# Kernel optimization log

Measured on AMD Instinct MI355X. Metric: run time of the kernel, lower is better.

Reference implementation:

```python
import jax, jax.numpy as jnp
import numpy as np
import math

B, I, O, SEG = 128, 2048, 2048, 10

def setup_inputs() -> dict:
    key = jax.random.key(0)
    k1, k2, k3, k4 = jax.random.split(key, 4)
    scale = 1.0 / math.sqrt(I)
    return {
        "x": jax.random.normal(k1, (B, I), dtype=jnp.float32),
        "context": jax.random.normal(k2, (O,), dtype=jnp.float32),
        "prev_activation": jax.random.normal(k3, (B, O), dtype=jnp.float32),
        "weight": jax.random.normal(k4, (O, I), dtype=jnp.float32) * scale,
        "bias": jnp.zeros((O,), dtype=jnp.float32),
        "astrocyte_activation": jnp.ones((O,), dtype=jnp.float32),
        "dendrite_segments": jax.random.normal(jax.random.fold_in(key, 7), (O, I, SEG), dtype=jnp.float32) * scale,
    }

def reference(x, context, prev_activation, weight, bias, astrocyte_activation, dendrite_segments):
    # Astrocyte gating of the linear weight: sigmoid(astro * context) -> [o]
    astro_mod = jax.nn.sigmoid(astrocyte_activation * context)
    # Dendritic branch: relu(einsum('bi,oij->boj')) summed over segments -> [b, o]
    dendritic_out = jnp.maximum(jnp.einsum('bi,oij->boj', x, dendrite_segments), 0.0).sum(axis=2)
    # Gated linear: F.linear(x, weight * astro_mod[:, None], bias) -> [b, o]
    out = x @ (weight * astro_mod[:, None]).T + bias
    # Note: torch's STDP/Hebbian weight mutations (synaptic_tag, protein_synthesis,
    # homeostatic scaling) occur AFTER 'out' is computed and do not affect the
    # returned tensor; they are pure parameter side effects, so omitted here.
    return out + dendritic_out
```

## Files before the change

### kernel.cpp

```cpp
#include <hip/hip_runtime.h>
#include <hip/hip_bf16.h>

#define B_ 128
#define I_ 2048
#define O_ 2048
#define SEG 10
#define BK 64
#define NST (I_ / BK)
#define XTILE 16384
#define DCH 2560
#define DLS 2816

typedef __attribute__((ext_vector_type(8))) short bf16x8;
typedef __attribute__((ext_vector_type(4))) float f32x4;

static __device__ __forceinline__ unsigned short f2bf(float f) {
    unsigned u = __float_as_uint(f);
    u += 0x7FFFu + ((u >> 16) & 1u);
    return (unsigned short)(u >> 16);
}

#define GLDS16(SRC, DST) \
    __builtin_amdgcn_global_load_lds( \
        (const __attribute__((address_space(1))) unsigned*)(SRC), \
        (__attribute__((address_space(3))) unsigned*)(DST), 16, 0, 0)
#define GLDS4(SRC, DST) \
    __builtin_amdgcn_global_load_lds( \
        (const __attribute__((address_space(1))) unsigned*)(SRC), \
        (__attribute__((address_space(3))) unsigned*)(DST), 4, 0, 0)

__global__ void xconv(const float* __restrict__ x, char* __restrict__ xb) {
    int idx = blockIdx.x * 256 + threadIdx.x;
    int row = idx >> 8;
    int c   = idx & 255;
    int k0  = c * 8;
    int t   = k0 >> 6;
    int kl  = k0 & 63;

    const float* xp = x + (size_t)row * I_ + k0;
    float4 a = *reinterpret_cast<const float4*>(xp);
    float4 b = *reinterpret_cast<const float4*>(xp + 4);

    bf16x8 h;
    h[0] = (short)f2bf(a.x); h[1] = (short)f2bf(a.y);
    h[2] = (short)f2bf(a.z); h[3] = (short)f2bf(a.w);
    h[4] = (short)f2bf(b.x); h[5] = (short)f2bf(b.y);
    h[6] = (short)f2bf(b.z); h[7] = (short)f2bf(b.w);

    size_t off = (size_t)t * XTILE + row * 128 + ((kl * 2) ^ ((row & 7) << 4));
    *reinterpret_cast<bf16x8*>(xb + off) = h;
}

__global__ __launch_bounds__(256, 2) void neuro_fused(
    const char*  __restrict__ xb,
    const float* __restrict__ ctx,
    const float* __restrict__ w,
    const float* __restrict__ bias,
    const float* __restrict__ astro,
    const float* __restrict__ D,
    float* __restrict__ out)
{
    __shared__ __align__(16) char xs[2][XTILE];
    __shared__ __align__(16) char dls[4][2][DLS];

    const int tid  = threadIdx.x;
    const int wave = tid >> 6;
    const int lane = tid & 63;
    const int o    = blockIdx.x * 4 + wave;
    const int col  = lane & 15;
    const int g    = lane >> 4;

    f32x4 acc[8];
#pragma unroll
    for (int m = 0; m < 8; ++m) acc[m] = (f32x4){0.f, 0.f, 0.f, 0.f};

    float am = astro[o] * ctx[o];
    am = 1.0f / (1.0f + __expf(-am));
    const float bo = bias[o];

    const int   fbase = (col < 10) ? col * 4 : DCH;
    const int   fstr  = (col < 10) ? 40 : 4;
    const float dmask = (col <= 10) ? 1.0f : 0.0f;
    const int   sw    = (col & 7) << 4;

    auto stage_x = [&](int t, int buf) {
        const char* src = xb + (size_t)t * XTILE + wave * 4096 + lane * 16;
        char* dst = &xs[buf][wave * 4096];
#pragma unroll
        for (int c = 0; c < 4; ++c)
            GLDS16(src + c * 1024, dst + c * 1024);
    };

    auto stage_d = [&](int t, int buf) {
        const char* srcD = (const char*)D + (size_t)o * (I_ * SEG * 4) + (size_t)t * DCH;
        char* dst = &dls[wave][buf][0];
#pragma unroll
        for (int c = 0; c < 2; ++c)
            GLDS16(srcD + c * 1024 + lane * 16, dst + c * 1024);
#pragma unroll
        for (int c = 0; c < 2; ++c)
            GLDS4(srcD + 2048 + c * 256 + lane * 4, dst + 2048 + c * 256);
        const char* srcW = (const char*)w + (size_t)o * (I_ * 4) + t * (BK * 4);
        GLDS4(srcW + lane * 4, dst + DCH);
    };

    auto compute = [&](int buf) {
        const char* dbase = &dls[wave][buf][0];
        const char* xbase = &xs[buf][0];
#pragma unroll
        for (int kk = 0; kk < 2; ++kk) {
            const char* fp = dbase + fbase + (32 * kk + 8 * g) * fstr;
            bf16x8 bfrag;
#pragma unroll
            for (int e = 0; e < 8; ++e) {
                float v = *reinterpret_cast<const float*>(fp + e * fstr);
                bfrag[e] = (short)f2bf(v * dmask);
            }
            const int kswz = (64 * kk + 16 * g) ^ sw;
#pragma unroll
            for (int m = 0; m < 8; ++m) {
                bf16x8 afrag = *reinterpret_cast<const bf16x8*>(
                    xbase + (m * 16 + col) * 128 + kswz);
                acc[m] = __builtin_amdgcn_mfma_f32_16x16x32_bf16(afrag, bfrag, acc[m], 0, 0, 0);
            }
        }
    };

    stage_x(0, 0);
    stage_d(0, 0);
    __syncthreads();

#pragma unroll 1
    for (int t = 0; t < NST; t += 2) {
        stage_x(t + 1, 1);
        stage_d(t + 1, 1);
        compute(0);
        __syncthreads();

        if (t + 2 < NST) {
            stage_x(t + 2, 0);
            stage_d(t + 2, 0);
        }
        compute(1);
        __syncthreads();
    }

#pragma unroll
    for (int m = 0; m < 8; ++m) {
#pragma unroll
        for (int r = 0; r < 4; ++r) {
            float v = acc[m][r];
            float dend = (col < 10) ? fmaxf(v, 0.0f) : 0.0f;
#pragma unroll
            for (int s = 1; s < 16; s <<= 1)
                dend += __shfl_xor(dend, s, 64);
            float lin = __shfl(v, (lane & 48) | 10, 64);
            if (col == 0) {
                int b = m * 16 + g * 4 + r;
                out[(size_t)b * O_ + o] = dend + am * lin + bo;
            }
        }
    }
}

extern "C" void kernel_launch(void* const* d_in, const int* in_sizes, int n_in,
                              void* d_out, int out_size, void* d_ws, size_t ws_size,
                              hipStream_t stream) {
    const float* x     = (const float*)d_in[0];
    const float* ctx   = (const float*)d_in[1];
    const float* w     = (const float*)d_in[3];
    const float* bias  = (const float*)d_in[4];
    const float* astro = (const float*)d_in[5];
    const float* D     = (const float*)d_in[6];
    float* out = (float*)d_out;
    char* xb = (char*)d_ws;

    xconv<<<dim3(128), dim3(256), 0, stream>>>(x, xb);
    neuro_fused<<<dim3(O_ / 4), dim3(256), 0, stream>>>(xb, ctx, w, bias, astro, D, out);
}
```

Measured before the change: 51.88 us.

## Split K across wave pairs, each wave computing two outputs to reuse x fragments

Each block still covers 4 output neurons, but each wave now handles 2 neurons over half of the K dimension (split-K with 2 slices). A-fragments are loaded once per stage and reused across both neurons, and the two K-halves are combined through LDS at the end. The aim is fewer LDS reads of x per MFMA and a different memory-level parallelism pattern. In exchange the tile is halved to BK=32 with a new swizzle, the accumulator register count doubles, and a cross-wave reduction step is added.

```diff
diff --git a/kernel.cpp b/kernel.cpp
--- a/kernel.cpp
+++ b/kernel.cpp
@@ -5,11 +5,12 @@
 #define I_ 2048
 #define O_ 2048
 #define SEG 10
-#define BK 64
-#define NST (I_ / BK)
-#define XTILE 16384
-#define DCH 2560
-#define DLS 2816
+#define BK 32
+#define KSLICE 1024
+#define NST (KSLICE / BK)
+#define XTILE 8192
+#define DCH 1280
+#define DLS 1408
 
 typedef __attribute__((ext_vector_type(8))) short bf16x8;
 typedef __attribute__((ext_vector_type(4))) float f32x4;
@@ -34,8 +35,8 @@
     int row = idx >> 8;
     int c   = idx & 255;
     int k0  = c * 8;
-    int t   = k0 >> 6;
-    int kl  = k0 & 63;
+    int tt  = k0 >> 5;
+    int kl  = k0 & 31;
 
     const float* xp = x + (size_t)row * I_ + k0;
     float4 a = *reinterpret_cast<const float4*>(xp);
@@ -47,7 +48,8 @@
     h[4] = (short)f2bf(b.x); h[5] = (short)f2bf(b.y);
     h[6] = (short)f2bf(b.z); h[7] = (short)f2bf(b.w);
 
-    size_t off = (size_t)t * XTILE + row * 128 + ((kl * 2) ^ ((row & 7) << 4));
+    int sw = ((row >> 1) & 3) << 4;
+    size_t off = (size_t)tt * XTILE + row * 64 + ((kl * 2) ^ sw);
     *reinterpret_cast<bf16x8*>(xb + off) = h;
 }
 
@@ -60,69 +62,69 @@
     const float* __restrict__ D,
     float* __restrict__ out)
 {
-    __shared__ __align__(16) char xs[2][XTILE];
-    __shared__ __align__(16) char dls[4][2][DLS];
+    __shared__ __align__(16) char xs[2][2][XTILE];
+    __shared__ __align__(16) char dls[4][2][2][DLS];
 
     const int tid  = threadIdx.x;
     const int wave = tid >> 6;
     const int lane = tid & 63;
-    const int o    = blockIdx.x * 4 + wave;
+    const int p    = wave >> 1;
+    const int s    = wave & 1;
+    const int o0   = blockIdx.x * 4 + p * 2;
     const int col  = lane & 15;
     const int g    = lane >> 4;
 
-    f32x4 acc[8];
-#pragma unroll
-    for (int m = 0; m < 8; ++m) acc[m] = (f32x4){0.f, 0.f, 0.f, 0.f};
-
-    float am = astro[o] * ctx[o];
-    am = 1.0f / (1.0f + __expf(-am));
-    const float bo = bias[o];
+    f32x4 acc[2][8];
+#pragma unroll
+    for (int oo = 0; oo < 2; ++oo)
+#pragma unroll
+        for (int m = 0; m < 8; ++m) acc[oo][m] = (f32x4){0.f, 0.f, 0.f, 0.f};
 
     const int   fbase = (col < 10) ? col * 4 : DCH;
     const int   fstr  = (col < 10) ? 40 : 4;
     const float dmask = (col <= 10) ? 1.0f : 0.0f;
-    const int   sw    = (col & 7) << 4;
+    const int   sw    = ((col >> 1) & 3) << 4;
 
     auto stage_x = [&](int t, int buf) {
-        const char* src = xb + (size_t)t * XTILE + wave * 4096 + lane * 16;
-        char* dst = &xs[buf][wave * 4096];
+        const char* src = xb + (size_t)(s * NST + t) * XTILE + p * 4096 + lane * 16;
+        char* dst = &xs[s][buf][p * 4096];
 #pragma unroll
         for (int c = 0; c < 4; ++c)
             GLDS16(src + c * 1024, dst + c * 1024);
     };
 
     auto stage_d = [&](int t, int buf) {
-        const char* srcD = (const char*)D + (size_t)o * (I_ * SEG * 4) + (size_t)t * DCH;
-        char* dst = &dls[wave][buf][0];
-#pragma unroll
-        for (int c = 0; c < 2; ++c)
-            GLDS16(srcD + c * 1024 + lane * 16, dst + c * 1024);
-#pragma unroll
-        for (int c = 0; c < 2; ++c)
-            GLDS4(srcD + 2048 + c * 256 + lane * 4, dst + 2048 + c * 256);
-        const char* srcW = (const char*)w + (size_t)o * (I_ * 4) + t * (BK * 4);
-        GLDS4(srcW + lane * 4, dst + DCH);
+        const size_t krow = (size_t)(s * KSLICE + t * BK);
+#pragma unroll
+        for (int oo = 0; oo < 2; ++oo) {
+            const char* srcD = (const char*)D + ((size_t)(o0 + oo) * (I_ * SEG) + krow * SEG) * 4;
+            char* dst = &dls[wave][buf][oo][0];
+            GLDS16(srcD + lane * 16, dst);
+            GLDS4(srcD + 1024 + lane * 4, dst + 1024);
+            const char* srcW = (const char*)w + ((size_t)(o0 + oo) * I_ + krow) * 4;
+            if (lane < 32) GLDS4(srcW + lane * 4, dst + DCH);
+        }
     };
 
     auto compute = [&](int buf) {
-        const char* dbase = &dls[wave][buf][0];
-        const char* xbase = &xs[buf][0];
-#pragma unroll
-        for (int kk = 0; kk < 2; ++kk) {
-            const char* fp = dbase + fbase + (32 * kk + 8 * g) * fstr;
+        const char* xbase = &xs[s][buf][0];
+        bf16x8 af[8];
+#pragma unroll
+        for (int m = 0; m < 8; ++m)
+            af[m] = *reinterpret_cast<const bf16x8*>(
+                xbase + (m * 16 + col) * 64 + ((16 * g) ^ sw));
+#pragma unroll
+        for (int oo = 0; oo < 2; ++oo) {
+            const char* fp = &dls[wave][buf][oo][0] + fbase + (8 * g) * fstr;
             bf16x8 bfrag;
 #pragma unroll
             for (int e = 0; e < 8; ++e) {
                 float v = *reinterpret_cast<const float*>(fp + e * fstr);
                 bfrag[e] = (short)f2bf(v * dmask);
             }
-            const int kswz = (64 * kk + 16 * g) ^ sw;
-#pragma unroll
-            for (int m = 0; m < 8; ++m) {
-                bf16x8 afrag = *reinterpret_cast<const bf16x8*>(
-                    xbase + (m * 16 + col) * 128 + kswz);
-                acc[m] = __builtin_amdgcn_mfma_f32_16x16x32_bf16(afrag, bfrag, acc[m], 0, 0, 0);
-            }
+#pragma unroll
+            for (int m = 0; m < 8; ++m)
+                acc[oo][m] = __builtin_amdgcn_mfma_f32_16x16x32_bf16(af[m], bfrag, acc[oo][m], 0, 0, 0);
         }
     };
 
@@ -145,19 +147,37 @@
         __syncthreads();
     }
 
-#pragma unroll
-    for (int m = 0; m < 8; ++m) {
-#pragma unroll
-        for (int r = 0; r < 4; ++r) {
-            float v = acc[m][r];
-            float dend = (col < 10) ? fmaxf(v, 0.0f) : 0.0f;
-#pragma unroll
-            for (int s = 1; s < 16; s <<= 1)
-                dend += __shfl_xor(dend, s, 64);
-            float lin = __shfl(v, (lane & 48) | 10, 64);
-            if (col == 0) {
-                int b = m * 16 + g * 4 + r;
-                out[(size_t)b * O_ + o] = dend + am * lin + bo;
+    float* cs = reinterpret_cast<float*>(&xs[0][0][0]);
+    if (s == 1) {
+#pragma unroll
+        for (int oo = 0; oo < 2; ++oo)
+#pragma unroll
+            for (int m = 0; m < 8; ++m)
+                *reinterpret_cast<f32x4*>(cs + p * 4096 + (oo * 8 + m) * 256 + lane * 4) = acc[oo][m];
+    }
+    __syncthreads();
+    if (s == 0) {
+#pragma unroll
+        for (int oo = 0; oo < 2; ++oo) {
+            float am = astro[o0 + oo] * ctx[o0 + oo];
+            am = 1.0f / (1.0f + __expf(-am));
+            const float bo = bias[o0 + oo];
+#pragma unroll
+            for (int m = 0; m < 8; ++m) {
+                f32x4 other = *reinterpret_cast<const f32x4*>(cs + p * 4096 + (oo * 8 + m) * 256 + lane * 4);
+#pragma unroll
+                for (int r = 0; r < 4; ++r) {
+                    float v = acc[oo][m][r] + other[r];
+                    float dend = (col < 10) ? fmaxf(v, 0.0f) : 0.0f;
+#pragma unroll
+                    for (int sh = 1; sh < 16; sh <<= 1)
+                        dend += __shfl_xor(dend, sh, 64);
+                    float lin = __shfl(v, (lane & 48) | 10, 64);
+                    if (col == 0) {
+                        int b = m * 16 + g * 4 + r;
+                        out[(size_t)b * O_ + (o0 + oo)] = dend + am * lin + bo;
+                    }
+                }
             }
         }
     }
@@ -176,5 +196,5 @@
     char* xb = (char*)d_ws;
 
     xconv<<<dim3(128), dim3(256), 0, stream>>>(x, xb);
-    neuro_fused<<<dim3(O_ / 4), dim3(256), 0, stream>>>(xb, ctx, w, bias, astro, D, out);
-}
+    neuro_fused<<<dim3(512), dim3(256), 0, stream>>>(xb, ctx, w, bias, astro, D, out);
+}
```

After: 54.72 us. 1.05x slower.

## Pre-pack weight to bf16 and restructure D/x/w staging into separate pipelines

Applied to the files above, without the earlier changes.

Adds a wpack kernel that converts the linear weight to bf16 and interleaves four output rows per group, so the main kernel loads it with 16-byte async LDS copies instead of 4-byte ones. Dendrite segments are now staged in 5 KB chunks covering two K-steps, using only 16-byte copies, and the weight is staged once every four steps by a single wave. The main loop becomes one step per iteration with separate prefetch cadences for x, D and w. The cost is an extra kernel launch and a weight conversion pass on every call, plus a column-dependent branch when building the B fragment.

```diff
diff --git a/kernel.cpp b/kernel.cpp
--- a/kernel.cpp
+++ b/kernel.cpp
@@ -6,10 +6,10 @@
 #define O_ 2048
 #define SEG 10
 #define BK 64
-#define NST (I_ / BK)
+#define NT (I_ / BK)
+#define NSS (I_ / 128)
 #define XTILE 16384
-#define DCH 2560
-#define DLS 2816
+#define DSS 5120
 
 typedef __attribute__((ext_vector_type(8))) short bf16x8;
 typedef __attribute__((ext_vector_type(4))) float f32x4;
@@ -24,17 +24,13 @@
     __builtin_amdgcn_global_load_lds( \
         (const __attribute__((address_space(1))) unsigned*)(SRC), \
         (__attribute__((address_space(3))) unsigned*)(DST), 16, 0, 0)
-#define GLDS4(SRC, DST) \
-    __builtin_amdgcn_global_load_lds( \
-        (const __attribute__((address_space(1))) unsigned*)(SRC), \
-        (__attribute__((address_space(3))) unsigned*)(DST), 4, 0, 0)
 
 __global__ void xconv(const float* __restrict__ x, char* __restrict__ xb) {
     int idx = blockIdx.x * 256 + threadIdx.x;
     int row = idx >> 8;
     int c   = idx & 255;
     int k0  = c * 8;
-    int t   = k0 >> 6;
+    int tt  = k0 >> 6;
     int kl  = k0 & 63;
 
     const float* xp = x + (size_t)row * I_ + k0;
@@ -47,21 +43,38 @@
     h[4] = (short)f2bf(b.x); h[5] = (short)f2bf(b.y);
     h[6] = (short)f2bf(b.z); h[7] = (short)f2bf(b.w);
 
-    size_t off = (size_t)t * XTILE + row * 128 + ((kl * 2) ^ ((row & 7) << 4));
+    size_t off = (size_t)tt * XTILE + row * 128 + ((kl * 2) ^ ((row & 7) << 4));
     *reinterpret_cast<bf16x8*>(xb + off) = h;
+}
+
+__global__ void wpack(const float* __restrict__ w, char* __restrict__ wp) {
+    int idx = blockIdx.x * 256 + threadIdx.x;
+    int grp = idx >> 10;
+    int kc2 = idx & 1023;
+
+    bf16x8 h;
+#pragma unroll
+    for (int ol = 0; ol < 4; ++ol) {
+        float2 v = *reinterpret_cast<const float2*>(
+            w + ((size_t)(grp * 4 + ol)) * I_ + kc2 * 2);
+        h[ol]     = (short)f2bf(v.x);
+        h[4 + ol] = (short)f2bf(v.y);
+    }
+    *reinterpret_cast<bf16x8*>(wp + (size_t)grp * 16384 + kc2 * 16) = h;
 }
 
 __global__ __launch_bounds__(256, 2) void neuro_fused(
     const char*  __restrict__ xb,
+    const char*  __restrict__ wp,
     const float* __restrict__ ctx,
-    const float* __restrict__ w,
     const float* __restrict__ bias,
     const float* __restrict__ astro,
     const float* __restrict__ D,
     float* __restrict__ out)
 {
     __shared__ __align__(16) char xs[2][XTILE];
-    __shared__ __align__(16) char dls[4][2][DLS];
+    __shared__ __align__(16) char dD[4][2][DSS];
+    __shared__ __align__(16) char wb[2][2048];
 
     const int tid  = threadIdx.x;
     const int wave = tid >> 6;
@@ -78,71 +91,83 @@
     am = 1.0f / (1.0f + __expf(-am));
     const float bo = bias[o];
 
-    const int   fbase = (col < 10) ? col * 4 : DCH;
-    const int   fstr  = (col < 10) ? 40 : 4;
-    const float dmask = (col <= 10) ? 1.0f : 0.0f;
-    const int   sw    = (col & 7) << 4;
-
-    auto stage_x = [&](int t, int buf) {
+    const char* Dbase = (const char*)D + (size_t)o * (I_ * SEG * 4);
+    const int sw = (col & 7) << 4;
+
+    auto stage_x = [&](int t) {
         const char* src = xb + (size_t)t * XTILE + wave * 4096 + lane * 16;
-        char* dst = &xs[buf][wave * 4096];
+        char* dst = &xs[t & 1][wave * 4096];
 #pragma unroll
         for (int c = 0; c < 4; ++c)
             GLDS16(src + c * 1024, dst + c * 1024);
     };
 
-    auto stage_d = [&](int t, int buf) {
-        const char* srcD = (const char*)D + (size_t)o * (I_ * SEG * 4) + (size_t)t * DCH;
-        char* dst = &dls[wave][buf][0];
-#pragma unroll
-        for (int c = 0; c < 2; ++c)
-            GLDS16(srcD + c * 1024 + lane * 16, dst + c * 1024);
-#pragma unroll
-        for (int c = 0; c < 2; ++c)
-            GLDS4(srcD + 2048 + c * 256 + lane * 4, dst + 2048 + c * 256);
-        const char* srcW = (const char*)w + (size_t)o * (I_ * 4) + t * (BK * 4);
-        GLDS4(srcW + lane * 4, dst + DCH);
-    };
-
-    auto compute = [&](int buf) {
-        const char* dbase = &dls[wave][buf][0];
-        const char* xbase = &xs[buf][0];
+    auto stage_D = [&](int S) {
+        const char* src = Dbase + (size_t)S * DSS + lane * 16;
+        char* dst = &dD[wave][S & 1][0];
+#pragma unroll
+        for (int c = 0; c < 5; ++c)
+            GLDS16(src + c * 1024, dst + c * 1024);
+    };
+
+    auto stage_w = [&](int g4) {
+        if (wave == (g4 & 3)) {
+            const char* src = wp + (size_t)blockIdx.x * 16384 + g4 * 2048 + lane * 16;
+            char* dst = &wb[g4 & 1][0];
+            GLDS16(src, dst);
+            GLDS16(src + 1024, dst + 1024);
+        }
+    };
+
+    auto compute = [&](int t) {
+        const char* xbase = &xs[t & 1][0];
+        const char* dbase = &dD[wave][(t >> 1) & 1][(t & 1) * 2560];
+        const char* wbase = &wb[(t >> 2) & 1][0];
 #pragma unroll
         for (int kk = 0; kk < 2; ++kk) {
-            const char* fp = dbase + fbase + (32 * kk + 8 * g) * fstr;
             bf16x8 bfrag;
-#pragma unroll
-            for (int e = 0; e < 8; ++e) {
-                float v = *reinterpret_cast<const float*>(fp + e * fstr);
-                bfrag[e] = (short)f2bf(v * dmask);
+            if (col < 10) {
+                const char* fp = dbase + kk * 1280 + (8 * g) * 40 + col * 4;
+#pragma unroll
+                for (int e = 0; e < 8; ++e)
+                    bfrag[e] = (short)f2bf(*reinterpret_cast<const float*>(fp + e * 40));
+            } else if (col == 10) {
+                const char* fp = wbase + ((t & 3) * 64 + kk * 32 + 8 * g) * 8 + wave * 2;
+#pragma unroll
+                for (int e = 0; e < 8; ++e)
+                    bfrag[e] = *reinterpret_cast<const short*>(fp + e * 8);
+            } else {
+#pragma unroll
+                for (int e = 0; e < 8; ++e) bfrag[e] = 0;
             }
-            const int kswz = (64 * kk + 16 * g) ^ sw;
+            const int kswz = (kk * 64 + 16 * g) ^ sw;
 #pragma unroll
             for (int m = 0; m < 8; ++m) {
-                bf16x8 afrag = *reinterpret_cast<const bf16x8*>(
+                bf16x8 af = *reinterpret_cast<const bf16x8*>(
                     xbase + (m * 16 + col) * 128 + kswz);
-                acc[m] = __builtin_amdgcn_mfma_f32_16x16x32_bf16(afrag, bfrag, acc[m], 0, 0, 0);
+                acc[m] = __builtin_amdgcn_mfma_f32_16x16x32_bf16(af, bfrag, acc[m], 0, 0, 0);
             }
         }
     };
 
-    stage_x(0, 0);
-    stage_d(0, 0);
-    __syncthreads();
+    stage_x(0); stage_x(1);
+    stage_D(0); stage_D(1);
+    stage_w(0); stage_w(1);
 
 #pragma unroll 1
-    for (int t = 0; t < NST; t += 2) {
-        stage_x(t + 1, 1);
-        stage_d(t + 1, 1);
-        compute(0);
+    for (int t = 0; t < NT; ++t) {
         __syncthreads();
-
-        if (t + 2 < NST) {
-            stage_x(t + 2, 0);
-            stage_d(t + 2, 0);
-        }
-        compute(1);
+        compute(t);
         __syncthreads();
+        if (t + 2 < NT) stage_x(t + 2);
+        if ((t & 1) == 1) {
+            int S = t >> 1;
+            if (S + 2 < NSS) stage_D(S + 2);
+        }
+        if ((t & 3) == 3) {
+            int g4 = t >> 2;
+            if (g4 + 2 < 8) stage_w(g4 + 2);
+        }
     }
 
 #pragma unroll
@@ -152,8 +177,8 @@
             float v = acc[m][r];
             float dend = (col < 10) ? fmaxf(v, 0.0f) : 0.0f;
 #pragma unroll
-            for (int s = 1; s < 16; s <<= 1)
-                dend += __shfl_xor(dend, s, 64);
+            for (int sh = 1; sh < 16; sh <<= 1)
+                dend += __shfl_xor(dend, sh, 64);
             float lin = __shfl(v, (lane & 48) | 10, 64);
             if (col == 0) {
                 int b = m * 16 + g * 4 + r;
@@ -173,8 +198,11 @@
     const float* astro = (const float*)d_in[5];
     const float* D     = (const float*)d_in[6];
     float* out = (float*)d_out;
+
     char* xb = (char*)d_ws;
+    char* wpk = (char*)d_ws + 524288;
 
     xconv<<<dim3(128), dim3(256), 0, stream>>>(x, xb);
-    neuro_fused<<<dim3(O_ / 4), dim3(256), 0, stream>>>(xb, ctx, w, bias, astro, D, out);
-}
+    wpack<<<dim3(2048), dim3(256), 0, stream>>>(w, wpk);
+    neuro_fused<<<dim3(512), dim3(256), 0, stream>>>(xb, wpk, ctx, bias, astro, D, out);
+}
```

After: 63.57 us. 22.5% more time.
